# Kernel optimization log

Hardware: AMD Instinct MI355X
Metric: run time of the kernel (lower is better)

Reference implementation:

```python
import jax, jax.numpy as jnp
import numpy as np
import math

NUM_HEADS = 16
WINDOW = 128  # telephone/sliding-window size: attend to self + previous WINDOW-1 tokens
EPS = 1e-6


def setup_inputs() -> dict:
    key = jax.random.key(0)
    k1, k2, k3, k4 = jax.random.split(key, 4)
    B, S, D = 4, 4096, 1024
    x = jax.random.normal(k1, (B, S, D), dtype=jnp.float32)
    g = jnp.ones((D,), dtype=jnp.float32)  # RMSNorm weight
    Wqkv = jax.random.normal(k2, (D, 3 * D), dtype=jnp.float32) * 0.02
    Wo = jax.random.normal(k3, (D, D), dtype=jnp.float32) * 0.02
    return {"x": x, "g": g, "Wqkv": Wqkv, "Wo": Wo}


def _telephone_block(x, g, Wqkv, Wo):
    B, S, D = x.shape
    H, dh, W = NUM_HEADS, D // NUM_HEADS, WINDOW
    nb = S // W  # number of key/query blocks

    # pre-RMSNorm
    xn = x * jax.lax.rsqrt(jnp.mean(x * x, axis=-1, keepdims=True) + EPS) * g

    # fused QKV projection
    qkv = xn @ Wqkv  # [B,S,3D]
    q, k, v = jnp.split(qkv, 3, axis=-1)

    def split_heads(t):
        # [B,S,D] -> [B,H,nb,W,dh]
        return t.reshape(B, nb, W, H, dh).transpose(0, 3, 1, 2, 4)

    q, k, v = split_heads(q), split_heads(k), split_heads(v)

    def shift_prev(t):
        # previous block of keys/values (zeros for block 0, masked below)
        return jnp.pad(t[:, :, :-1], ((0, 0), (0, 0), (1, 0), (0, 0), (0, 0)))

    k_ext = jnp.concatenate([shift_prev(k), k], axis=3)  # [B,H,nb,2W,dh]
    v_ext = jnp.concatenate([shift_prev(v), v], axis=3)

    scale = 1.0 / math.sqrt(dh)
    scores = jnp.einsum('bhnqd,bhnkd->bhnqk', q, k_ext) * scale  # [B,H,nb,W,2W]

    # sliding-window causal mask within the [prev-block, cur-block] key span.
    # query local pos i in [0,W); key extended pos j in [0,2W) maps to offset j-W.
    i = jnp.arange(W)[:, None]
    j = jnp.arange(2 * W)[None, :]
    base = (j > i) & (j <= i + W)          # last W tokens incl. self
    first = base & (j >= W)                # block 0 has no previous block
    blk0 = (jnp.arange(nb) == 0)[:, None, None]
    mask = jnp.where(blk0, first[None], base[None])  # [nb,W,2W]

    scores = jnp.where(mask[None, None], scores, jnp.finfo(scores.dtype).min)
    p = jax.nn.softmax(scores, axis=-1)
    o = jnp.einsum('bhnqk,bhnkd->bhnqd', p, v_ext)   # [B,H,nb,W,dh]
    o = o.transpose(0, 2, 3, 1, 4).reshape(B, S, D)
    h = o @ Wo
    return x + h  # residual


def reference(x, g, Wqkv, Wo):
    return _telephone_block(x, g, Wqkv, Wo)
```

## Files before the change

kernel.cpp:

```cpp
#include <hip/hip_runtime.h>
#include <hip/hip_bf16.h>


typedef __attribute__((ext_vector_type(8))) short s8v;
typedef __attribute__((ext_vector_type(4))) float f4v;

#define MFMA_BF16(A, B, C) __builtin_amdgcn_mfma_f32_16x16x32_bf16((A), (B), (C), 0, 0, 0)

static __device__ __forceinline__ void gload_lds16(const void* g, void* l) {
    __builtin_amdgcn_global_load_lds((const __attribute__((address_space(1))) void*)g,
                                     (__attribute__((address_space(3))) void*)l, 16, 0, 0);
}

static __device__ __forceinline__ unsigned short f2bf(float f) {
    return __builtin_bit_cast(unsigned short, __float2bfloat16(f));
}

__global__ __launch_bounds__(256) void transpose_cast_kernel(const float* __restrict__ in,
                                                             unsigned short* __restrict__ out,
                                                             int K, int N) {
    __shared__ float tile[32][33];
    int nbk = K >> 5;
    int bk = blockIdx.x % nbk;
    int bn = blockIdx.x / nbk;
    int tx = threadIdx.x & 31, ty = threadIdx.x >> 5;
#pragma unroll
    for (int i = 0; i < 4; i++) {
        int r = ty + i * 8;
        tile[r][tx] = in[(size_t)(bk * 32 + r) * N + bn * 32 + tx];
    }
    __syncthreads();
#pragma unroll
    for (int i = 0; i < 4; i++) {
        int r = ty + i * 8;
        out[(size_t)(bn * 32 + r) * K + bk * 32 + tx] = f2bf(tile[tx][r]);
    }
}

__global__ __launch_bounds__(256) void rmsnorm_kernel(const float* __restrict__ x,
                                                      const float* __restrict__ g,
                                                      unsigned short* __restrict__ xn) {
    const int D = 1024;
    int row = blockIdx.x;
    int t = threadIdx.x;
    float4 v = ((const float4*)(x + (size_t)row * D))[t];
    float ss = v.x * v.x + v.y * v.y + v.z * v.z + v.w * v.w;
#pragma unroll
    for (int off = 32; off >= 1; off >>= 1) ss += __shfl_xor(ss, off, 64);
    __shared__ float partials[4];
    if ((t & 63) == 0) partials[t >> 6] = ss;
    __syncthreads();
    float tot = partials[0] + partials[1] + partials[2] + partials[3];
    float scale = rsqrtf(tot * (1.0f / D) + 1e-6f);
    float4 gv = ((const float4*)g)[t];
    ushort4 o;
    o.x = f2bf(v.x * scale * gv.x);
    o.y = f2bf(v.y * scale * gv.y);
    o.z = f2bf(v.z * scale * gv.z);
    o.w = f2bf(v.w * scale * gv.w);
    ((ushort4*)xn)[(size_t)row * (D / 4) + t] = o;
}

template <int MODE>
__global__ __launch_bounds__(512, 2) void gemm256_kernel(const unsigned short* __restrict__ A,
                                                         const unsigned short* __restrict__ Bt,
                                                         unsigned short* __restrict__ Cb,
                                                         float* __restrict__ Cf,
                                                         const float* __restrict__ resid,
                                                         int M, int N, int K) {
    __shared__ __align__(16) char lds_s[131072];

    const int nbn = N >> 8;
    const int nwg = (M >> 8) * nbn;
    int bid = blockIdx.x;
    int cpx = nwg >> 3;
    int wg = (bid & 7) * cpx + (bid >> 3);
    int bm = wg / nbn, bn = wg % nbn;

    int tid = threadIdx.x, lane = tid & 63, w = tid >> 6;
    int wm = w >> 2, wn = w & 3;
    int hl = lane >> 4, ll = lane & 15;

    const unsigned short* Ab = A + (size_t)bm * 256 * K;
    const unsigned short* Bb = Bt + (size_t)bn * 256 * K;

    int srow = lane >> 3;
    int scol = ((lane & 7) ^ srow) * 8;

    int c0 = (hl * 16) ^ ((ll & 7) * 16);
    const char* ldsA0 = lds_s + wm * 16384 + ll * 128 + c0;
    const char* ldsA1 = lds_s + wm * 16384 + ll * 128 + (c0 ^ 64);
    const char* ldsB0 = lds_s + 32768 + (wn >> 1) * 16384 + ((wn & 1) * 64 + ll) * 128 + c0;
    const char* ldsB1 = lds_s + 32768 + (wn >> 1) * 16384 + ((wn & 1) * 64 + ll) * 128 + (c0 ^ 64);

    const int NT = K >> 6;

    f4v acc[8][4] = {};
    s8v bfr[4][2];

#define STAGE(t_, isB_, h_) do {                                                          \
        int te_ = (t_) < NT ? (t_) : (t_)-NT;                                             \
        const unsigned short* g_ = ((isB_) ? Bb : Ab)                                     \
            + (size_t)((h_)*128 + srow) * K + te_ * 64 + scol;                            \
        char* l_ = lds_s + (((t_)&1) * 65536 + (isB_)*32768 + (h_)*16384);                \
        gload_lds16(g_ + (size_t)(w * 8) * K, l_ + w * 1024);                             \
        gload_lds16(g_ + (size_t)(64 + w * 8) * K, l_ + 8192 + w * 1024);                 \
    } while (0)

#define PHASE(buf_, p4_, st_, sb_, sh_, dv_) do {                                         \
        s8v a0k0 = *(const s8v*)(ldsA0 + (buf_)*65536 + (2 * (p4_)) * 2048);              \
        s8v a0k1 = *(const s8v*)(ldsA1 + (buf_)*65536 + (2 * (p4_)) * 2048);              \
        s8v a1k0 = *(const s8v*)(ldsA0 + (buf_)*65536 + (2 * (p4_) + 1) * 2048);          \
        s8v a1k1 = *(const s8v*)(ldsA1 + (buf_)*65536 + (2 * (p4_) + 1) * 2048);          \
        if ((p4_) == 0) {                                                                 \
            _Pragma("unroll") for (int n = 0; n < 4; n++) {                               \
                bfr[n][0] = *(const s8v*)(ldsB0 + (buf_)*65536 + n * 2048);               \
                bfr[n][1] = *(const s8v*)(ldsB1 + (buf_)*65536 + n * 2048);               \
            }                                                                             \
        }                                                                                 \
        STAGE(st_, sb_, sh_);                                                             \
        if (dv_) asm volatile("s_waitcnt vmcnt(4)" ::: "memory");                         \
        asm volatile("s_barrier" ::: "memory");                                           \
        asm volatile("s_waitcnt lgkmcnt(0)" ::: "memory");                                \
        __builtin_amdgcn_s_setprio(1);                                                    \
        _Pragma("unroll") for (int n = 0; n < 4; n++) {                                   \
            acc[2 * (p4_)][n] = MFMA_BF16(a0k0, bfr[n][0], acc[2 * (p4_)][n]);            \
            acc[2 * (p4_)][n] = MFMA_BF16(a0k1, bfr[n][1], acc[2 * (p4_)][n]);            \
            acc[2 * (p4_) + 1][n] = MFMA_BF16(a1k0, bfr[n][0], acc[2 * (p4_) + 1][n]);    \
            acc[2 * (p4_) + 1][n] = MFMA_BF16(a1k1, bfr[n][1], acc[2 * (p4_) + 1][n]);    \
        }                                                                                 \
        __builtin_amdgcn_s_setprio(0);                                                    \
        asm volatile("s_barrier" ::: "memory");                                           \
    } while (0)

    STAGE(0, 0, 0); STAGE(0, 0, 1); STAGE(0, 1, 0); STAGE(0, 1, 1);
    STAGE(1, 1, 0); STAGE(1, 1, 1);
    asm volatile("s_waitcnt vmcnt(4)" ::: "memory");
    asm volatile("s_barrier" ::: "memory");

    for (int i = 0; i < NT / 2; i++) {
        int t1 = 2 * i + 1;
        PHASE(0, 0, t1, 0, 0, 0);
        PHASE(0, 1, t1, 0, 1, 0);
        PHASE(0, 2, t1 + 1, 1, 0, 0);
        PHASE(0, 3, t1 + 1, 1, 1, 1);
        PHASE(1, 0, t1 + 1, 0, 0, 0);
        PHASE(1, 1, t1 + 1, 0, 1, 0);
        PHASE(1, 2, t1 + 2, 1, 0, 0);
        PHASE(1, 3, t1 + 2, 1, 1, 1);
    }
#undef PHASE
#undef STAGE

    int crow0 = bm * 256 + wm * 128;
    int ccol0 = bn * 256 + wn * 64;
#pragma unroll
    for (int m = 0; m < 8; m++) {
#pragma unroll
        for (int r = 0; r < 4; r++) {
            int row = crow0 + m * 16 + hl * 4 + r;
#pragma unroll
            for (int n = 0; n < 4; n++) {
                int col = ccol0 + n * 16 + ll;
                float val = acc[m][n][r];
                if (MODE == 0) {
                    Cb[(size_t)row * N + col] = f2bf(val);
                } else {
                    size_t idx = (size_t)row * N + col;
                    Cf[idx] = resid[idx] + val;
                }
            }
        }
    }
}

__global__ __launch_bounds__(256, 3) void attn_kernel(const unsigned short* __restrict__ qkv,
                                                      unsigned short* __restrict__ obuf) {
    constexpr int S = 4096, D = 1024, H = 16, W = 128, NB = 32;
    constexpr int TD = 3 * D;
    constexpr int PS = 40;

    __shared__ __align__(16) char smem[44032];
    unsigned short* KV = (unsigned short*)smem;

    int bid = blockIdx.x;
    int blk = bid % NB;
    int h = (bid / NB) % H;
    int b = bid / (NB * H);

    int tid = threadIdx.x, lane = tid & 63, w = tid >> 6;
    int hl = lane >> 4, ll = lane & 15;
    unsigned short* Ps = (unsigned short*)(smem + 33792) + w * 32 * PS;

    int kbase = blk * W - W;
    size_t rowbase = (size_t)(b * S);

    {
        int lr = lane >> 3;
        int scb = ((lane & 7) ^ lr) * 16;
#pragma unroll
        for (int r = 0; r < 8; r++) {
            int row = r * 32 + w * 8 + lr;
            int s = kbase + row;
            s = s < 0 ? 0 : s;
            const char* src = (const char*)(qkv + (rowbase + s) * TD + D + h * 64) + scb;
            char* dst = smem + (size_t)(r * 32 + w * 8) * 128 + lane * 16;
            gload_lds16(src, dst);
        }
    }

    s8v qf[2][2];
    {
        const unsigned short* qb = qkv + (rowbase + blk * W + w * 32) * TD + h * 64;
#pragma unroll
        for (int mf = 0; mf < 2; mf++)
#pragma unroll
            for (int ks = 0; ks < 2; ks++)
                qf[mf][ks] = *(const s8v*)(qb + (size_t)(mf * 16 + ll) * TD + ks * 32 + hl * 8);
    }

    s8v vreg[8];
    {
        int k0 = w * 64 + (lane >> 3) * 8;
        int d0 = (lane & 7) * 8;
#pragma unroll
        for (int it = 0; it < 8; it++) {
            int s = kbase + k0 + it;
            s = s < 0 ? 0 : s;
            vreg[it] = *(const s8v*)(qkv + (rowbase + s) * TD + 2 * D + h * 64 + d0);
        }
    }
    __syncthreads();

    f4v sc[2][9] = {};
    int g0 = w * 2;
    __builtin_amdgcn_s_setprio(1);
#pragma unroll
    for (int gi = 0; gi < 10; gi++) {
#pragma unroll
        for (int ks = 0; ks < 2; ks++) {
            int row = (g0 + gi) * 16 + ll;
            s8v kf = *(const s8v*)(smem + (size_t)row * 128 +
                                   (((unsigned)(ks * 64 + hl * 16)) ^ ((ll & 7) << 4)));
            if (gi < 9) sc[0][gi] = MFMA_BF16(qf[0][ks], kf, sc[0][gi]);
            if (gi > 0) sc[1][gi - 1] = MFMA_BF16(qf[1][ks], kf, sc[1][gi - 1]);
        }
    }
    __builtin_amdgcn_s_setprio(0);

    float linv[2][4];
#pragma unroll
    for (int mf = 0; mf < 2; mf++) {
#pragma unroll
        for (int r = 0; r < 4; r++) {
            int ip = hl * 4 + r;
            float mx = -1e30f;
#pragma unroll
            for (int nf = 0; nf < 9; nf++) {
                bool ok = (nf > 0 || ll > ip) && (nf < 8 || ll <= ip) &&
                          (blk > 0 || (g0 + mf + nf) >= 8);
                float sval = ok ? sc[mf][nf][r] * 0.125f : -1e30f;
                sc[mf][nf][r] = sval;
                mx = fmaxf(mx, sval);
            }
#pragma unroll
            for (int off = 1; off < 16; off <<= 1) mx = fmaxf(mx, __shfl_xor(mx, off, 64));
            float sum = 0.f;
#pragma unroll
            for (int nf = 0; nf < 9; nf++) {
                float p = __expf(sc[mf][nf][r] - mx);
                sc[mf][nf][r] = p;
                sum += p;
            }
#pragma unroll
            for (int off = 1; off < 16; off <<= 1) sum += __shfl_xor(sum, off, 64);
            linv[mf][r] = 1.f / sum;
        }
    }

    __syncthreads();

    {
        int k0 = w * 64 + (lane >> 3) * 8;
        int d0 = (lane & 7) * 8;
#pragma unroll
        for (int e = 0; e < 8; e++) {
            int d = d0 + e;
            s8v tmp;
#pragma unroll
            for (int i = 0; i < 8; i++) tmp[i] = vreg[i][e];
            *(s8v*)(KV + d * 264 + (k0 ^ (((d >> 3) & 7) << 3))) = tmp;
        }
    }
    __syncthreads();

    f4v o[2][4] = {};
#pragma unroll
    for (int c = 0; c < 5; c++) {
#pragma unroll
        for (int mf = 0; mf < 2; mf++) {
#pragma unroll
            for (int j16 = 0; j16 < 2; j16++) {
                int nf = c * 2 + j16 - mf;
                int nfc = nf < 0 ? 0 : (nf > 8 ? 8 : nf);
#pragma unroll
                for (int r = 0; r < 4; r++) {
                    float val = (nf >= 0 && nf < 9) ? sc[mf][nfc][r] : 0.f;
                    Ps[(mf * 16 + hl * 4 + r) * PS + j16 * 16 + ll] = f2bf(val);
                }
            }
        }
        asm volatile("s_waitcnt lgkmcnt(0)" ::: "memory");
        s8v pa[2];
        pa[0] = *(const s8v*)(Ps + ll * PS + hl * 8);
        pa[1] = *(const s8v*)(Ps + (16 + ll) * PS + hl * 8);
        int cb = (w + c) * 32;
        __builtin_amdgcn_s_setprio(1);
#pragma unroll
        for (int nd = 0; nd < 4; nd++) {
            int d = nd * 16 + ll;
            int kk = (cb + hl * 8) ^ (((d >> 3) & 7) << 3);
            s8v vb = *(const s8v*)(KV + d * 264 + kk);
            o[0][nd] = MFMA_BF16(pa[0], vb, o[0][nd]);
            o[1][nd] = MFMA_BF16(pa[1], vb, o[1][nd]);
        }
        __builtin_amdgcn_s_setprio(0);
    }

    unsigned short* ob = obuf + (rowbase + blk * W + w * 32) * D + h * 64;
#pragma unroll
    for (int mf = 0; mf < 2; mf++)
#pragma unroll
        for (int r = 0; r < 4; r++) {
            int row = mf * 16 + hl * 4 + r;
#pragma unroll
            for (int nd = 0; nd < 4; nd++)
                ob[(size_t)row * D + nd * 16 + ll] = f2bf(o[mf][nd][r] * linv[mf][r]);
        }
}

extern "C" void kernel_launch(void* const* d_in, const int* in_sizes, int n_in,
                              void* d_out, int out_size, void* d_ws, size_t ws_size,
                              hipStream_t stream) {
    const float* x = (const float*)d_in[0];
    const float* g = (const float*)d_in[1];
    const float* Wqkv = (const float*)d_in[2];
    const float* Wo = (const float*)d_in[3];
    float* out = (float*)d_out;

    const int S = 4096, D = 1024, B = 4;
    const int M = B * S;
    const int N3 = 3 * D;

    char* ws = (char*)d_ws;
    unsigned short* WqkvT = (unsigned short*)ws;
    unsigned short* WoT = (unsigned short*)(ws + 6291456);
    unsigned short* xn = (unsigned short*)(ws + 8388608);
    unsigned short* qkv = (unsigned short*)(ws + 41943040);

    transpose_cast_kernel<<<dim3((D / 32) * (N3 / 32)), dim3(256), 0, stream>>>(Wqkv, WqkvT, D, N3);
    transpose_cast_kernel<<<dim3((D / 32) * (D / 32)), dim3(256), 0, stream>>>(Wo, WoT, D, D);
    rmsnorm_kernel<<<dim3(M), dim3(256), 0, stream>>>(x, g, xn);
    gemm256_kernel<0><<<dim3((M / 256) * (N3 / 256)), dim3(512), 0, stream>>>(
        xn, WqkvT, qkv, nullptr, nullptr, M, N3, D);
    attn_kernel<<<dim3(B * 16 * (S / 128)), dim3(256), 0, stream>>>(qkv, xn);
    gemm256_kernel<1><<<dim3((M / 256) * (D / 256)), dim3(512), 0, stream>>>(
        xn, WoT, nullptr, out, x, M, D, D);
}
```

Measured before the change: 208.0 us.

## Process two query blocks per attention workgroup sharing overlapping K/V loads

The attention kernel now handles two consecutive 128-token query blocks per 512-thread workgroup. It loads 384 K/V rows once instead of 256 rows twice, so the shared previous/current block is fetched only once. The two weight transpose-cast launches are also merged into a single launch. In exchange, LDS use per block rises to about 70KB and occupancy is limited to two blocks per CU.

New measurement: 220.7 us. 1.06x slower.

```diff
diff --git a/kernel.cpp b/kernel.cpp
--- a/kernel.cpp
+++ b/kernel.cpp
@@ -16,13 +16,24 @@
     return __builtin_bit_cast(unsigned short, __float2bfloat16(f));
 }
 
-__global__ __launch_bounds__(256) void transpose_cast_kernel(const float* __restrict__ in,
-                                                             unsigned short* __restrict__ out,
-                                                             int K, int N) {
+__global__ __launch_bounds__(256) void transpose_cast_kernel(const float* __restrict__ Wqkv,
+                                                             unsigned short* __restrict__ WqkvT,
+                                                             const float* __restrict__ Wo,
+                                                             unsigned short* __restrict__ WoT) {
+    const int K = 1024;
+    int nb1 = (K >> 5) * (3072 >> 5);
+    const float* in;
+    unsigned short* out;
+    int N, bidx;
+    if (blockIdx.x < (unsigned)nb1) {
+        in = Wqkv; out = WqkvT; N = 3072; bidx = blockIdx.x;
+    } else {
+        in = Wo; out = WoT; N = 1024; bidx = blockIdx.x - nb1;
+    }
     __shared__ float tile[32][33];
     int nbk = K >> 5;
-    int bk = blockIdx.x % nbk;
-    int bn = blockIdx.x / nbk;
+    int bk = bidx % nbk;
+    int bn = bidx / nbk;
     int tx = threadIdx.x & 31, ty = threadIdx.x >> 5;
 #pragma unroll
     for (int i = 0; i < 4; i++) {
@@ -174,44 +185,46 @@
     }
 }
 
-__global__ __launch_bounds__(256, 3) void attn_kernel(const unsigned short* __restrict__ qkv,
+__global__ __launch_bounds__(512, 2) void attn_kernel(const unsigned short* __restrict__ qkv,
                                                       unsigned short* __restrict__ obuf) {
-    constexpr int S = 4096, D = 1024, H = 16, W = 128, NB = 32;
+    constexpr int S = 4096, D = 1024, H = 16, W = 128, NP = 16;
     constexpr int TD = 3 * D;
-    constexpr int PS = 40;
-
-    __shared__ __align__(16) char smem[44032];
+    constexpr int PS = 40, VS = 392;
+
+    __shared__ __align__(16) char smem[71680];
     unsigned short* KV = (unsigned short*)smem;
 
     int bid = blockIdx.x;
-    int blk = bid % NB;
-    int h = (bid / NB) % H;
-    int b = bid / (NB * H);
+    int bp = bid % NP;
+    int h = (bid / NP) % H;
+    int b = bid / (NP * H);
 
     int tid = threadIdx.x, lane = tid & 63, w = tid >> 6;
+    int g = w >> 2, wl = w & 3;
     int hl = lane >> 4, ll = lane & 15;
-    unsigned short* Ps = (unsigned short*)(smem + 33792) + w * 32 * PS;
-
-    int kbase = blk * W - W;
+    unsigned short* Ps = (unsigned short*)(smem + 51200) + w * 32 * PS;
+
+    int kb0 = bp * 2 * W - W;
+    int blk_g = bp * 2 + g;
     size_t rowbase = (size_t)(b * S);
 
     {
         int lr = lane >> 3;
         int scb = ((lane & 7) ^ lr) * 16;
 #pragma unroll
-        for (int r = 0; r < 8; r++) {
-            int row = r * 32 + w * 8 + lr;
-            int s = kbase + row;
+        for (int r = 0; r < 6; r++) {
+            int row = r * 64 + w * 8 + lr;
+            int s = kb0 + row;
             s = s < 0 ? 0 : s;
             const char* src = (const char*)(qkv + (rowbase + s) * TD + D + h * 64) + scb;
-            char* dst = smem + (size_t)(r * 32 + w * 8) * 128 + lane * 16;
+            char* dst = smem + (size_t)(r * 64 + w * 8) * 128 + lane * 16;
             gload_lds16(src, dst);
         }
     }
 
     s8v qf[2][2];
     {
-        const unsigned short* qb = qkv + (rowbase + blk * W + w * 32) * TD + h * 64;
+        const unsigned short* qb = qkv + (rowbase + blk_g * W + wl * 32) * TD + h * 64;
 #pragma unroll
         for (int mf = 0; mf < 2; mf++)
 #pragma unroll
@@ -220,26 +233,27 @@
     }
 
     s8v vreg[8];
-    {
-        int k0 = w * 64 + (lane >> 3) * 8;
-        int d0 = (lane & 7) * 8;
+    int vkblk = tid >> 3;
+    int vd0 = (tid & 7) * 8;
+    if (vkblk < 48) {
+        int k0 = vkblk * 8;
 #pragma unroll
         for (int it = 0; it < 8; it++) {
-            int s = kbase + k0 + it;
+            int s = kb0 + k0 + it;
             s = s < 0 ? 0 : s;
-            vreg[it] = *(const s8v*)(qkv + (rowbase + s) * TD + 2 * D + h * 64 + d0);
+            vreg[it] = *(const s8v*)(qkv + (rowbase + s) * TD + 2 * D + h * 64 + vd0);
         }
     }
     __syncthreads();
 
     f4v sc[2][9] = {};
-    int g0 = w * 2;
+    int g0 = wl * 2;
     __builtin_amdgcn_s_setprio(1);
 #pragma unroll
     for (int gi = 0; gi < 10; gi++) {
 #pragma unroll
         for (int ks = 0; ks < 2; ks++) {
-            int row = (g0 + gi) * 16 + ll;
+            int row = g * 128 + (g0 + gi) * 16 + ll;
             s8v kf = *(const s8v*)(smem + (size_t)row * 128 +
                                    (((unsigned)(ks * 64 + hl * 16)) ^ ((ll & 7) << 4)));
             if (gi < 9) sc[0][gi] = MFMA_BF16(qf[0][ks], kf, sc[0][gi]);
@@ -258,7 +272,7 @@
 #pragma unroll
             for (int nf = 0; nf < 9; nf++) {
                 bool ok = (nf > 0 || ll > ip) && (nf < 8 || ll <= ip) &&
-                          (blk > 0 || (g0 + mf + nf) >= 8);
+                          (blk_g > 0 || (g0 + mf + nf) >= 8);
                 float sval = ok ? sc[mf][nf][r] * 0.125f : -1e30f;
                 sc[mf][nf][r] = sval;
                 mx = fmaxf(mx, sval);
@@ -280,16 +294,15 @@
 
     __syncthreads();
 
-    {
-        int k0 = w * 64 + (lane >> 3) * 8;
-        int d0 = (lane & 7) * 8;
+    if (vkblk < 48) {
+        int k0 = vkblk * 8;
 #pragma unroll
         for (int e = 0; e < 8; e++) {
-            int d = d0 + e;
+            int d = vd0 + e;
             s8v tmp;
 #pragma unroll
             for (int i = 0; i < 8; i++) tmp[i] = vreg[i][e];
-            *(s8v*)(KV + d * 264 + (k0 ^ (((d >> 3) & 7) << 3))) = tmp;
+            *(s8v*)(KV + d * VS + (k0 ^ (((d >> 3) & 7) << 3))) = tmp;
         }
     }
     __syncthreads();
@@ -314,20 +327,20 @@
         s8v pa[2];
         pa[0] = *(const s8v*)(Ps + ll * PS + hl * 8);
         pa[1] = *(const s8v*)(Ps + (16 + ll) * PS + hl * 8);
-        int cb = (w + c) * 32;
+        int cb = g * 128 + (wl + c) * 32;
         __builtin_amdgcn_s_setprio(1);
 #pragma unroll
         for (int nd = 0; nd < 4; nd++) {
             int d = nd * 16 + ll;
             int kk = (cb + hl * 8) ^ (((d >> 3) & 7) << 3);
-            s8v vb = *(const s8v*)(KV + d * 264 + kk);
+            s8v vb = *(const s8v*)(KV + d * VS + kk);
             o[0][nd] = MFMA_BF16(pa[0], vb, o[0][nd]);
             o[1][nd] = MFMA_BF16(pa[1], vb, o[1][nd]);
         }
         __builtin_amdgcn_s_setprio(0);
     }
 
-    unsigned short* ob = obuf + (rowbase + blk * W + w * 32) * D + h * 64;
+    unsigned short* ob = obuf + (rowbase + blk_g * W + wl * 32) * D + h * 64;
 #pragma unroll
     for (int mf = 0; mf < 2; mf++)
 #pragma unroll
@@ -358,12 +371,12 @@
     unsigned short* xn = (unsigned short*)(ws + 8388608);
     unsigned short* qkv = (unsigned short*)(ws + 41943040);
 
-    transpose_cast_kernel<<<dim3((D / 32) * (N3 / 32)), dim3(256), 0, stream>>>(Wqkv, WqkvT, D, N3);
-    transpose_cast_kernel<<<dim3((D / 32) * (D / 32)), dim3(256), 0, stream>>>(Wo, WoT, D, D);
+    transpose_cast_kernel<<<dim3((D / 32) * (N3 / 32) + (D / 32) * (D / 32)), dim3(256), 0,
+                            stream>>>(Wqkv, WqkvT, Wo, WoT);
     rmsnorm_kernel<<<dim3(M), dim3(256), 0, stream>>>(x, g, xn);
     gemm256_kernel<0><<<dim3((M / 256) * (N3 / 256)), dim3(512), 0, stream>>>(
         xn, WqkvT, qkv, nullptr, nullptr, M, N3, D);
-    attn_kernel<<<dim3(B * 16 * (S / 128)), dim3(256), 0, stream>>>(qkv, xn);
+    attn_kernel<<<dim3(B * 16 * (S / 128 / 2)), dim3(512), 0, stream>>>(qkv, xn);
     gemm256_kernel<1><<<dim3((M / 256) * (D / 256)), dim3(512), 0, stream>>>(
         xn, WoT, nullptr, out, x, M, D, D);
 }
```
